# Optimization experiments

Hardware: AMD Instinct MI355X
Metric: run time of the kernel (lower is better)

## Reference

```python
import jax, jax.numpy as jnp
import numpy as np

TOP_K = 2
NUM_EXPERTS = 8
D_MODEL = 1024


def setup_inputs() -> dict:
    key = jax.random.key(0)
    kx, kw, kb = jax.random.split(key, 3)
    x = jax.random.normal(kx, (8, 4096, D_MODEL), dtype=jnp.float32)
    bound = 1.0 / np.sqrt(D_MODEL)
    W = jax.random.uniform(kw, (NUM_EXPERTS, D_MODEL), dtype=jnp.float32, minval=-bound, maxval=bound)
    b = jax.random.uniform(kb, (NUM_EXPERTS,), dtype=jnp.float32, minval=-bound, maxval=bound)
    return {"x": x, "W": W, "b": b}


def reference(x, W, b):
    # logits: [B, S, E]
    logits = jnp.einsum('bsd,ed->bse', x, W) + b
    values, indices = jax.lax.top_k(logits, TOP_K)  # [B,S,K]
    # softmax over a tensor that is -inf everywhere except top-k positions
    # == softmax over the top-k values, scattered back; non-selected experts get 0.
    topk_w = jax.nn.softmax(values, axis=-1)  # [B,S,K]
    one_hot = jax.nn.one_hot(indices, NUM_EXPERTS, dtype=logits.dtype)  # [B,S,K,E]
    weights = jnp.einsum('bsk,bske->bse', topk_w, one_hot)
    return weights, indices
```

## Files before the change

### kernel.cpp

```cpp
#include <hip/hip_runtime.h>
#include <math.h>

#define D_MODEL 1024
#define NUM_EXPERTS 8
#define TOP_K 2
#define LANES_PER_TOKEN 8
#define TOKENS_PER_WAVE 8
#define WAVES_PER_BLOCK 4
#define TOKENS_PER_BLOCK (TOKENS_PER_WAVE * WAVES_PER_BLOCK)

typedef float f4 __attribute__((ext_vector_type(4)));

__global__ __launch_bounds__(256) void gating_kernel(
    const float* __restrict__ x, const float* __restrict__ W,
    const float* __restrict__ b, float* __restrict__ out_w,
    float* __restrict__ out_idx, int n_tokens)
{
    __shared__ float Wlds[NUM_EXPERTS * D_MODEL];

    {
        const f4* Wg = (const f4*)W;
        f4* Ws = (f4*)Wlds;
        const int tid = threadIdx.x;
#pragma unroll
        for (int i = 0; i < (NUM_EXPERTS * D_MODEL / 4) / 256; ++i)
            Ws[tid + i * 256] = Wg[tid + i * 256];
    }
    __syncthreads();

    const int wave = threadIdx.x >> 6;
    const int lane = threadIdx.x & 63;
    const int g = lane >> 3;
    const int l = lane & 7;
    const int token = blockIdx.x * TOKENS_PER_BLOCK + wave * TOKENS_PER_WAVE + g;
    if (token >= n_tokens) return;

    const f4* xg = (const f4*)x + (size_t)token * (D_MODEL / 4) + l;
    const f4* Wl = (const f4*)Wlds + l;

    float acc[NUM_EXPERTS];
#pragma unroll
    for (int e = 0; e < NUM_EXPERTS; ++e) acc[e] = 0.f;

#pragma unroll
    for (int c = 0; c < 4; ++c) {
        f4 xa[8];
#pragma unroll
        for (int kk = 0; kk < 8; ++kk)
            xa[kk] = __builtin_nontemporal_load(xg + (c * 8 + kk) * 8);
#pragma unroll
        for (int e = 0; e < NUM_EXPERTS; ++e) {
            float s = acc[e];
#pragma unroll
            for (int kk = 0; kk < 8; ++kk) {
                const f4 wv = Wl[e * 256 + (c * 8 + kk) * 8];
                s += xa[kk].x * wv.x + xa[kk].y * wv.y +
                     xa[kk].z * wv.z + xa[kk].w * wv.w;
            }
            acc[e] = s;
        }
    }

#pragma unroll
    for (int e = 0; e < NUM_EXPERTS; ++e) {
        float v = acc[e];
        v += __shfl_xor(v, 1, 64);
        v += __shfl_xor(v, 2, 64);
        v += __shfl_xor(v, 4, 64);
        acc[e] = v + b[e];
    }

    float v0 = -INFINITY, v1 = -INFINITY;
    int i0 = 0, i1 = 0;
#pragma unroll
    for (int e = 0; e < NUM_EXPERTS; ++e) {
        float v = acc[e];
        if (v > v0) { v1 = v0; i1 = i0; v0 = v; i0 = e; }
        else if (v > v1) { v1 = v; i1 = e; }
    }
    const float e1 = expf(v1 - v0);
    const float w0 = 1.f / (1.f + e1);
    const float w1 = e1 * w0;

    if (l < 2) {
        const int base = l * 4;
        f4 v4;
        v4.x = (base + 0 == i0) ? w0 : ((base + 0 == i1) ? w1 : 0.f);
        v4.y = (base + 1 == i0) ? w0 : ((base + 1 == i1) ? w1 : 0.f);
        v4.z = (base + 2 == i0) ? w0 : ((base + 2 == i1) ? w1 : 0.f);
        v4.w = (base + 3 == i0) ? w0 : ((base + 3 == i1) ? w1 : 0.f);
        ((f4*)(out_w + (size_t)token * NUM_EXPERTS))[l] = v4;
    } else if (l == 2) {
        *(float2*)(out_idx + (size_t)token * TOP_K) =
            make_float2((float)i0, (float)i1);
    }
}

extern "C" void kernel_launch(void* const* d_in, const int* in_sizes, int n_in,
                              void* d_out, int out_size, void* d_ws, size_t ws_size,
                              hipStream_t stream) {
    const float* x = (const float*)d_in[0];
    const float* W = (const float*)d_in[1];
    const float* b = (const float*)d_in[2];
    float* out = (float*)d_out;

    const int n_tokens = in_sizes[0] / D_MODEL;
    float* out_w   = out;
    float* out_idx = out + (size_t)n_tokens * NUM_EXPERTS;

    const int grid = (n_tokens + TOKENS_PER_BLOCK - 1) / TOKENS_PER_BLOCK;
    gating_kernel<<<grid, 256, 0, stream>>>(x, W, b, out_w, out_idx, n_tokens);
}
```

Baseline: 185.5 us.

## Compute four tokens per 16-lane group with double-buffered x loads

Each 16-lane group now computes four tokens at once, so every W value read from LDS is reused across four tokens instead of one. This cuts LDS traffic per FLOP. The x loads are software double-buffered in 8 chunks so the next chunk's global loads are issued while the current chunk is being computed. The costs are more registers for 32 accumulators plus two buffers, fewer waves in flight, and an extra shuffle step in the reduction. Tokens per block doubles, which halves the grid.

```diff
diff --git a/kernel.cpp b/kernel.cpp
--- a/kernel.cpp
+++ b/kernel.cpp
@@ -4,8 +4,9 @@
 #define D_MODEL 1024
 #define NUM_EXPERTS 8
 #define TOP_K 2
-#define LANES_PER_TOKEN 8
-#define TOKENS_PER_WAVE 8
+#define LPG 16
+#define GTOK 4
+#define TOKENS_PER_WAVE 16
 #define WAVES_PER_BLOCK 4
 #define TOKENS_PER_BLOCK (TOKENS_PER_WAVE * WAVES_PER_BLOCK)
 
@@ -30,51 +31,73 @@
 
     const int wave = threadIdx.x >> 6;
     const int lane = threadIdx.x & 63;
-    const int g = lane >> 3;
-    const int l = lane & 7;
-    const int token = blockIdx.x * TOKENS_PER_BLOCK + wave * TOKENS_PER_WAVE + g;
-    if (token >= n_tokens) return;
+    const int g = lane >> 4;
+    const int l = lane & 15;
+    const int tok0 = blockIdx.x * TOKENS_PER_BLOCK + wave * TOKENS_PER_WAVE + g * GTOK;
+    if (tok0 >= n_tokens) return;
 
-    const f4* xg = (const f4*)x + (size_t)token * (D_MODEL / 4) + l;
-    const f4* Wl = (const f4*)Wlds + l;
+    const f4* xb = (const f4*)x + (size_t)tok0 * (D_MODEL / 4) + l;
+    const f4* Wf = (const f4*)Wlds + l;
 
-    float acc[NUM_EXPERTS];
+    float acc[GTOK][NUM_EXPERTS];
 #pragma unroll
-    for (int e = 0; e < NUM_EXPERTS; ++e) acc[e] = 0.f;
+    for (int t = 0; t < GTOK; ++t)
+#pragma unroll
+        for (int e = 0; e < NUM_EXPERTS; ++e) acc[t][e] = 0.f;
+
+    f4 buf[2][GTOK * 2];
+#pragma unroll
+    for (int t = 0; t < GTOK; ++t)
+#pragma unroll
+        for (int j = 0; j < 2; ++j)
+            buf[0][t * 2 + j] = __builtin_nontemporal_load(xb + t * 256 + j * 16);
 
 #pragma unroll
-    for (int c = 0; c < 4; ++c) {
-        f4 xa[8];
+    for (int c = 0; c < 8; ++c) {
+        const int cur = c & 1, nxt = cur ^ 1;
+        if (c < 7) {
 #pragma unroll
-        for (int kk = 0; kk < 8; ++kk)
-            xa[kk] = __builtin_nontemporal_load(xg + (c * 8 + kk) * 8);
+            for (int t = 0; t < GTOK; ++t)
+#pragma unroll
+                for (int j = 0; j < 2; ++j)
+                    buf[nxt][t * 2 + j] = __builtin_nontemporal_load(
+                        xb + t * 256 + ((c + 1) * 2 + j) * 16);
+        }
 #pragma unroll
         for (int e = 0; e < NUM_EXPERTS; ++e) {
-            float s = acc[e];
 #pragma unroll
-            for (int kk = 0; kk < 8; ++kk) {
-                const f4 wv = Wl[e * 256 + (c * 8 + kk) * 8];
-                s += xa[kk].x * wv.x + xa[kk].y * wv.y +
-                     xa[kk].z * wv.z + xa[kk].w * wv.w;
+            for (int j = 0; j < 2; ++j) {
+                const f4 wv = Wf[e * 256 + (c * 2 + j) * 16];
+#pragma unroll
+                for (int t = 0; t < GTOK; ++t) {
+                    const f4 xv = buf[cur][t * 2 + j];
+                    acc[t][e] += xv.x * wv.x + xv.y * wv.y + xv.z * wv.z + xv.w * wv.w;
+                }
             }
-            acc[e] = s;
         }
     }
 
 #pragma unroll
-    for (int e = 0; e < NUM_EXPERTS; ++e) {
-        float v = acc[e];
-        v += __shfl_xor(v, 1, 64);
-        v += __shfl_xor(v, 2, 64);
-        v += __shfl_xor(v, 4, 64);
-        acc[e] = v + b[e];
-    }
+    for (int t = 0; t < GTOK; ++t)
+#pragma unroll
+        for (int e = 0; e < NUM_EXPERTS; ++e) {
+            float v = acc[t][e];
+            v += __shfl_xor(v, 1, 64);
+            v += __shfl_xor(v, 2, 64);
+            v += __shfl_xor(v, 4, 64);
+            v += __shfl_xor(v, 8, 64);
+            acc[t][e] = v + b[e];
+        }
+
+    const int t = l >> 2;
+    const int r = l & 3;
+    const int token = tok0 + t;
 
     float v0 = -INFINITY, v1 = -INFINITY;
     int i0 = 0, i1 = 0;
 #pragma unroll
     for (int e = 0; e < NUM_EXPERTS; ++e) {
-        float v = acc[e];
+        float v = acc[t][e];
         if (v > v0) { v1 = v0; i1 = i0; v0 = v; i0 = e; }
         else if (v > v1) { v1 = v; i1 = e; }
     }
@@ -82,15 +105,15 @@
     const float w0 = 1.f / (1.f + e1);
     const float w1 = e1 * w0;
 
-    if (l < 2) {
-        const int base = l * 4;
+    if (r < 2) {
+        const int base = r * 4;
         f4 v4;
         v4.x = (base + 0 == i0) ? w0 : ((base + 0 == i1) ? w1 : 0.f);
         v4.y = (base + 1 == i0) ? w0 : ((base + 1 == i1) ? w1 : 0.f);
         v4.z = (base + 2 == i0) ? w0 : ((base + 2 == i1) ? w1 : 0.f);
         v4.w = (base + 3 == i0) ? w0 : ((base + 3 == i1) ? w1 : 0.f);
-        ((f4*)(out_w + (size_t)token * NUM_EXPERTS))[l] = v4;
-    } else if (l == 2) {
+        ((f4*)(out_w + (size_t)token * NUM_EXPERTS))[r] = v4;
+    } else if (r == 2) {
         *(float2*)(out_idx + (size_t)token * TOP_K) =
             make_float2((float)i0, (float)i1);
     }
```

Result: slower. 199.3 us (+7.4%).

## Map lane groups to experts and drop LDS staging of gating weights

Applied to the files above, without the earlier changes.

Each lane group of a wave now owns one expert and computes it for 8 tokens, reading W straight from global memory instead of staging the full 32KB weight matrix in shared memory per block. Partial dot products are reduced with shuffles, written to a small LDS scratch, and one lane per token then does top-2, softmax and the output writes. The aim is to remove the per-block W copy and the heavy LDS traffic and occupancy limit it caused. In exchange, every x vector is loaded by all 8 expert groups, which raises the number of vector memory instructions roughly eightfold. The change also adds a block-wide barrier and a launch-bounds occupancy hint.

```diff
diff --git a/kernel.cpp b/kernel.cpp
--- a/kernel.cpp
+++ b/kernel.cpp
@@ -4,95 +4,100 @@
 #define D_MODEL 1024
 #define NUM_EXPERTS 8
 #define TOP_K 2
-#define LANES_PER_TOKEN 8
-#define TOKENS_PER_WAVE 8
+#define TPW 8
 #define WAVES_PER_BLOCK 4
-#define TOKENS_PER_BLOCK (TOKENS_PER_WAVE * WAVES_PER_BLOCK)
+#define TOKENS_PER_BLOCK (TPW * WAVES_PER_BLOCK)
 
 typedef float f4 __attribute__((ext_vector_type(4)));
 
-__global__ __launch_bounds__(256) void gating_kernel(
+__global__ __launch_bounds__(256, 4) void gating_kernel(
     const float* __restrict__ x, const float* __restrict__ W,
     const float* __restrict__ b, float* __restrict__ out_w,
     float* __restrict__ out_idx, int n_tokens)
 {
-    __shared__ float Wlds[NUM_EXPERTS * D_MODEL];
-
-    {
-        const f4* Wg = (const f4*)W;
-        f4* Ws = (f4*)Wlds;
-        const int tid = threadIdx.x;
-#pragma unroll
-        for (int i = 0; i < (NUM_EXPERTS * D_MODEL / 4) / 256; ++i)
-            Ws[tid + i * 256] = Wg[tid + i * 256];
-    }
-    __syncthreads();
+    __shared__ float scratch[WAVES_PER_BLOCK][NUM_EXPERTS][TPW];
 
     const int wave = threadIdx.x >> 6;
     const int lane = threadIdx.x & 63;
-    const int g = lane >> 3;
-    const int l = lane & 7;
-    const int token = blockIdx.x * TOKENS_PER_BLOCK + wave * TOKENS_PER_WAVE + g;
-    if (token >= n_tokens) return;
+    const int e = lane >> 3;
+    const int s = lane & 7;
+    const int tok0 = blockIdx.x * TOKENS_PER_BLOCK + wave * TPW;
 
-    const f4* xg = (const f4*)x + (size_t)token * (D_MODEL / 4) + l;
-    const f4* Wl = (const f4*)Wlds + l;
+    const f4* Wf = (const f4*)(W + (size_t)e * D_MODEL);
+    const f4* xf = (const f4*)(x + (size_t)tok0 * D_MODEL);
 
-    float acc[NUM_EXPERTS];
+    float acc[TPW];
 #pragma unroll
-    for (int e = 0; e < NUM_EXPERTS; ++e) acc[e] = 0.f;
+    for (int t = 0; t < TPW; ++t) acc[t] = 0.f;
 
 #pragma unroll
-    for (int c = 0; c < 4; ++c) {
-        f4 xa[8];
+    for (int p = 0; p < 8; ++p) {
+        f4 wv[4];
 #pragma unroll
-        for (int kk = 0; kk < 8; ++kk)
-            xa[kk] = __builtin_nontemporal_load(xg + (c * 8 + kk) * 8);
+        for (int j = 0; j < 4; ++j) wv[j] = Wf[p * 32 + j * 8 + s];
 #pragma unroll
-        for (int e = 0; e < NUM_EXPERTS; ++e) {
-            float s = acc[e];
+        for (int t = 0; t < TPW; ++t) {
+            f4 xv[4];
 #pragma unroll
-            for (int kk = 0; kk < 8; ++kk) {
-                const f4 wv = Wl[e * 256 + (c * 8 + kk) * 8];
-                s += xa[kk].x * wv.x + xa[kk].y * wv.y +
-                     xa[kk].z * wv.z + xa[kk].w * wv.w;
-            }
-            acc[e] = s;
+            for (int j = 0; j < 4; ++j)
+                xv[j] = __builtin_nontemporal_load(xf + t * 256 + p * 32 + j * 8 + s);
+#pragma unroll
+            for (int j = 0; j < 4; ++j)
+                acc[t] += xv[j].x * wv[j].x + xv[j].y * wv[j].y +
+                          xv[j].z * wv[j].z + xv[j].w * wv[j].w;
         }
     }
 
 #pragma unroll
-    for (int e = 0; e < NUM_EXPERTS; ++e) {
-        float v = acc[e];
+    for (int t = 0; t < TPW; ++t) {
+        float v = acc[t];
         v += __shfl_xor(v, 1, 64);
         v += __shfl_xor(v, 2, 64);
         v += __shfl_xor(v, 4, 64);
-        acc[e] = v + b[e];
+        acc[t] = v;
     }
 
-    float v0 = -INFINITY, v1 = -INFINITY;
-    int i0 = 0, i1 = 0;
+    if (s == 0) {
 #pragma unroll
-    for (int e = 0; e < NUM_EXPERTS; ++e) {
-        float v = acc[e];
-        if (v > v0) { v1 = v0; i1 = i0; v0 = v; i0 = e; }
-        else if (v > v1) { v1 = v; i1 = e; }
+        for (int t = 0; t < TPW; ++t) scratch[wave][e][t] = acc[t];
     }
-    const float e1 = expf(v1 - v0);
-    const float w0 = 1.f / (1.f + e1);
-    const float w1 = e1 * w0;
+    __syncthreads();
 
-    if (l < 2) {
-        const int base = l * 4;
-        f4 v4;
-        v4.x = (base + 0 == i0) ? w0 : ((base + 0 == i1) ? w1 : 0.f);
-        v4.y = (base + 1 == i0) ? w0 : ((base + 1 == i1) ? w1 : 0.f);
-        v4.z = (base + 2 == i0) ? w0 : ((base + 2 == i1) ? w1 : 0.f);
-        v4.w = (base + 3 == i0) ? w0 : ((base + 3 == i1) ? w1 : 0.f);
-        ((f4*)(out_w + (size_t)token * NUM_EXPERTS))[l] = v4;
-    } else if (l == 2) {
-        *(float2*)(out_idx + (size_t)token * TOP_K) =
-            make_float2((float)i0, (float)i1);
+    if (lane < TPW) {
+        const int token = tok0 + lane;
+        if (token < n_tokens) {
+            float lg[NUM_EXPERTS];
+#pragma unroll
+            for (int ee = 0; ee < NUM_EXPERTS; ++ee)
+                lg[ee] = scratch[wave][ee][lane] + b[ee];
+
+            float v0 = -INFINITY, v1 = -INFINITY;
+            int i0 = 0, i1 = 0;
+#pragma unroll
+            for (int ee = 0; ee < NUM_EXPERTS; ++ee) {
+                float v = lg[ee];
+                if (v > v0) { v1 = v0; i1 = i0; v0 = v; i0 = ee; }
+                else if (v > v1) { v1 = v; i1 = ee; }
+            }
+            const float e1 = expf(v1 - v0);
+            const float w0 = 1.f / (1.f + e1);
+            const float w1 = e1 * w0;
+
+            f4 o0, o1;
+            o0.x = (0 == i0) ? w0 : ((0 == i1) ? w1 : 0.f);
+            o0.y = (1 == i0) ? w0 : ((1 == i1) ? w1 : 0.f);
+            o0.z = (2 == i0) ? w0 : ((2 == i1) ? w1 : 0.f);
+            o0.w = (3 == i0) ? w0 : ((3 == i1) ? w1 : 0.f);
+            o1.x = (4 == i0) ? w0 : ((4 == i1) ? w1 : 0.f);
+            o1.y = (5 == i0) ? w0 : ((5 == i1) ? w1 : 0.f);
+            o1.z = (6 == i0) ? w0 : ((6 == i1) ? w1 : 0.f);
+            o1.w = (7 == i0) ? w0 : ((7 == i1) ? w1 : 0.f);
+            f4* dst = (f4*)(out_w + (size_t)token * NUM_EXPERTS);
+            dst[0] = o0;
+            dst[1] = o1;
+            *(float2*)(out_idx + (size_t)token * TOP_K) =
+                make_float2((float)i0, (float)i1);
+        }
     }
 }
 
```

Result: slower. 285.8 us (+54.0%).

## Drop LDS staging of gate weights and read W from cache with 16 lanes/token

Applied to the files above, without the earlier changes.

Removes the per-block copy of the full 32KB weight matrix into shared memory and the barrier that follows; each lane now reads its weight slices straight from global memory, relying on L1/L2 hits. Tokens are split across 16 lanes instead of 8, with an extra shuffle step in the reduction. The x stream is software-prefetched one chunk ahead, and launch bounds request 8 blocks per SM. This is meant to cut the redundant weight copy and the low occupancy caused by LDS use. The cost is more cache traffic for weights and fewer x loads in flight per thread.

```diff
diff --git a/kernel.cpp b/kernel.cpp
--- a/kernel.cpp
+++ b/kernel.cpp
@@ -4,61 +4,42 @@
 #define D_MODEL 1024
 #define NUM_EXPERTS 8
 #define TOP_K 2
-#define LANES_PER_TOKEN 8
-#define TOKENS_PER_WAVE 8
+#define TPW 4
 #define WAVES_PER_BLOCK 4
-#define TOKENS_PER_BLOCK (TOKENS_PER_WAVE * WAVES_PER_BLOCK)
+#define TOKENS_PER_BLOCK (TPW * WAVES_PER_BLOCK)
 
 typedef float f4 __attribute__((ext_vector_type(4)));
 
-__global__ __launch_bounds__(256) void gating_kernel(
+__global__ __launch_bounds__(256, 8) void gating_kernel(
     const float* __restrict__ x, const float* __restrict__ W,
     const float* __restrict__ b, float* __restrict__ out_w,
     float* __restrict__ out_idx, int n_tokens)
 {
-    __shared__ float Wlds[NUM_EXPERTS * D_MODEL];
-
-    {
-        const f4* Wg = (const f4*)W;
-        f4* Ws = (f4*)Wlds;
-        const int tid = threadIdx.x;
-#pragma unroll
-        for (int i = 0; i < (NUM_EXPERTS * D_MODEL / 4) / 256; ++i)
-            Ws[tid + i * 256] = Wg[tid + i * 256];
-    }
-    __syncthreads();
-
     const int wave = threadIdx.x >> 6;
     const int lane = threadIdx.x & 63;
-    const int g = lane >> 3;
-    const int l = lane & 7;
-    const int token = blockIdx.x * TOKENS_PER_BLOCK + wave * TOKENS_PER_WAVE + g;
+    const int t = lane >> 4;
+    const int l = lane & 15;
+    const int token = blockIdx.x * TOKENS_PER_BLOCK + wave * TPW + t;
     if (token >= n_tokens) return;
 
-    const f4* xg = (const f4*)x + (size_t)token * (D_MODEL / 4) + l;
-    const f4* Wl = (const f4*)Wlds + l;
+    const f4* xf = (const f4*)x + (size_t)token * (D_MODEL / 4) + l;
+    const f4* Wf = (const f4*)W + l;
 
     float acc[NUM_EXPERTS];
 #pragma unroll
     for (int e = 0; e < NUM_EXPERTS; ++e) acc[e] = 0.f;
 
+    f4 xc = __builtin_nontemporal_load(xf);
 #pragma unroll
-    for (int c = 0; c < 4; ++c) {
-        f4 xa[8];
-#pragma unroll
-        for (int kk = 0; kk < 8; ++kk)
-            xa[kk] = __builtin_nontemporal_load(xg + (c * 8 + kk) * 8);
+    for (int s = 0; s < 16; ++s) {
+        f4 xn;
+        if (s < 15) xn = __builtin_nontemporal_load(xf + (s + 1) * 16);
 #pragma unroll
         for (int e = 0; e < NUM_EXPERTS; ++e) {
-            float s = acc[e];
-#pragma unroll
-            for (int kk = 0; kk < 8; ++kk) {
-                const f4 wv = Wl[e * 256 + (c * 8 + kk) * 8];
-                s += xa[kk].x * wv.x + xa[kk].y * wv.y +
-                     xa[kk].z * wv.z + xa[kk].w * wv.w;
-            }
-            acc[e] = s;
+            const f4 wv = Wf[e * 256 + s * 16];
+            acc[e] += xc.x * wv.x + xc.y * wv.y + xc.z * wv.z + xc.w * wv.w;
         }
+        xc = xn;
     }
 
 #pragma unroll
@@ -67,6 +48,7 @@
         v += __shfl_xor(v, 1, 64);
         v += __shfl_xor(v, 2, 64);
         v += __shfl_xor(v, 4, 64);
+        v += __shfl_xor(v, 8, 64);
         acc[e] = v + b[e];
     }
 
```

Measured after the change: 217.4 us. +17.2%, slower.
